# Optimization experiments

Hardware: AMD Instinct MI355X
Metric: run time of the kernel (lower is better)

## Reference

```python
import jax, jax.numpy as jnp
import numpy as np

HEADS, DIM_HEAD, CHUNK, GROUPS, EPS = 4, 32, 2048, 8, 1e-5


def setup_inputs() -> dict:
    key = jax.random.key(0)
    ks = jax.random.split(key, 10)
    B, C, H, W = 1, 128, 128, 128
    inner = HEADS * DIM_HEAD  # 128
    s = 0.02
    return {
        "x": jax.random.normal(ks[0], (B, C, H, W), jnp.float32),
        "w_qkv": jax.random.normal(ks[1], (3 * inner, C), jnp.float32) * s,
        "se_w1": jax.random.normal(ks[2], (inner // 4, inner), jnp.float32) * s,
        "se_b1": jax.random.normal(ks[3], (inner // 4,), jnp.float32) * s,
        "se_w2": jax.random.normal(ks[4], (inner, inner // 4), jnp.float32) * s,
        "se_b2": jax.random.normal(ks[5], (inner,), jnp.float32) * s,
        "out_w": jax.random.normal(ks[6], (C, inner), jnp.float32) * s,
        "out_b": jax.random.normal(ks[7], (C,), jnp.float32) * s,
        "gn_w": 1.0 + jax.random.normal(ks[8], (C,), jnp.float32) * s,
        "gn_b": jax.random.normal(ks[9], (C,), jnp.float32) * s,
    }


def reference(x, w_qkv, se_w1, se_b1, se_w2, se_b2, out_w, out_b, gn_w, gn_b):
    B, C, H, W = x.shape
    inner = HEADS * DIM_HEAD
    hw = H * W
    nc = hw // CHUNK  # hw chosen divisible by CHUNK
    scale = DIM_HEAD ** -0.5

    # 1x1 conv to qkv (no bias)
    qkv = jnp.einsum('oc,bchw->bohw', w_qkv, x)  # [B, 3*inner, H, W]
    q, k, v = jnp.split(qkv.reshape(B, 3 * inner, hw), 3, axis=1)

    def to_blocks(t):  # [B, inner, hw] -> [B*heads, dh, nc, CHUNK]
        return t.reshape(B * HEADS, DIM_HEAD, nc, CHUNK)

    q, k, v = to_blocks(q), to_blocks(k), to_blocks(v)

    # block-diagonal attention: attn[n, j] = softmax_j(q[:, n]^T k[:, j])
    attn = jax.nn.softmax(jnp.einsum('bdnc,bdne->bnce', q, k) * scale, axis=-1)
    # chunk_out[d, j] = sum_c v[d, c] * attn[c, j]  (contracts the un-normalized axis, as in torch bmm(v, attn))
    out = jnp.einsum('bdnc,bncj->bdnj', v, attn).reshape(B, inner, H, W)

    # SE gating
    s = out.mean(axis=(2, 3))                       # [B, inner]
    s = jax.nn.silu(s @ se_w1.T + se_b1)            # [B, inner//4]
    g = jax.nn.sigmoid(s @ se_w2.T + se_b2)         # [B, inner]
    out = out * g[:, :, None, None]

    # output 1x1 conv + GroupNorm(8, C)
    y = jnp.einsum('oc,bchw->bohw', out_w, out) + out_b[None, :, None, None]
    yg = y.reshape(B, GROUPS, C // GROUPS, H, W)
    mu = yg.mean(axis=(2, 3, 4), keepdims=True)
    var = yg.var(axis=(2, 3, 4), keepdims=True)
    yn = ((yg - mu) * jax.lax.rsqrt(var + EPS)).reshape(B, C, H, W)
    return yn * gn_w[None, :, None, None] + gn_b[None, :, None, None]
```

## Files before the change

### kernel.cpp

```cpp
#include <hip/hip_runtime.h>
#include <hip/hip_bf16.h>

#define HW 16384
#define QSCALE (0.17677669529663687f * 1.4426950408889634f)

typedef __attribute__((ext_vector_type(8))) short short8;
typedef __attribute__((ext_vector_type(4))) float floatx4;
typedef __attribute__((ext_vector_type(16))) float floatx16;

__device__ inline unsigned cvt_pk_bf16(float a, float b) {
  unsigned r;
  asm("v_cvt_pk_bf16_f32 %0, %1, %2" : "=v"(r) : "v"(a), "v"(b));
  return r;
}
__device__ inline unsigned short f2bf(float a) {
  return (unsigned short)(cvt_pk_bf16(a, 0.f) & 0xffff);
}
__device__ inline float bf2f(unsigned short u) {
  union { unsigned u; float f; } c;
  c.u = (unsigned)u << 16;
  return c.f;
}
__device__ inline void permlane32_swap(unsigned& a, unsigned& b) {
  asm("v_permlane32_swap_b32 %0, %1" : "+v"(a), "+v"(b));
}

__global__ __launch_bounds__(256) void cast_w(
    const float* __restrict__ w, unsigned short* __restrict__ w_bf) {
  const int i4 = (blockIdx.x * 256 + threadIdx.x) * 4;
  const int o = i4 >> 7;
  const float sc = (o < 128) ? QSCALE : 1.f;
  float4 v = *(const float4*)&w[i4];
  uint2 u = {cvt_pk_bf16(v.x * sc, v.y * sc), cvt_pk_bf16(v.z * sc, v.w * sc)};
  *(uint2*)&w_bf[i4] = u;
}

__global__ __launch_bounds__(256) void cast_transpose_x(
    const float* __restrict__ x, unsigned short* __restrict__ x_t) {
  __shared__ float tile[128][65];
  const int p0 = blockIdx.x * 64;
  const int t = threadIdx.x;
  #pragma unroll
  for (int i = 0; i < 32; ++i) {
    int idx = t + i * 256;
    int c = idx >> 6, p = idx & 63;
    tile[c][p] = x[c * HW + p0 + p];
  }
  __syncthreads();
  const int p = t >> 2, q = t & 3;
  unsigned u[16];
  #pragma unroll
  for (int i = 0; i < 16; ++i)
    u[i] = cvt_pk_bf16(tile[q * 32 + 2 * i][p], tile[q * 32 + 2 * i + 1][p]);
  unsigned short* dst = &x_t[(p0 + p) * 128 + q * 32];
  #pragma unroll
  for (int i = 0; i < 4; ++i) *(uint4*)&dst[i * 8] = *(const uint4*)&u[i * 4];
}

__global__ __launch_bounds__(512) void gemm_qkv(
    const unsigned short* __restrict__ w_bf, const unsigned short* __restrict__ x_t,
    unsigned short* __restrict__ q_t, unsigned short* __restrict__ k_t,
    unsigned short* __restrict__ v_bf) {
  const int wave = threadIdx.x >> 6, lane = threadIdx.x & 63;
  const int lr = lane & 15, g = lane >> 4;
  const int p0 = blockIdx.x * 64;
  const int ow = wave * 48;
  const floatx4 zero = {0.f, 0.f, 0.f, 0.f};

  short8 a[3][4];
  #pragma unroll
  for (int mf = 0; mf < 3; ++mf)
    #pragma unroll
    for (int kk = 0; kk < 4; ++kk)
      a[mf][kk] = *(const short8*)&w_bf[(ow + mf * 16 + lr) * 128 + kk * 32 + g * 8];

  floatx4 acc[3][4];
  #pragma unroll
  for (int mf = 0; mf < 3; ++mf)
    #pragma unroll
    for (int nf = 0; nf < 4; ++nf) acc[mf][nf] = zero;

  #pragma unroll
  for (int kk = 0; kk < 4; ++kk) {
    #pragma unroll
    for (int nf = 0; nf < 4; ++nf) {
      short8 b = *(const short8*)&x_t[(p0 + nf * 16 + lr) * 128 + kk * 32 + g * 8];
      #pragma unroll
      for (int mf = 0; mf < 3; ++mf)
        acc[mf][nf] = __builtin_amdgcn_mfma_f32_16x16x32_bf16(a[mf][kk], b, acc[mf][nf], 0, 0, 0);
    }
  }

  #pragma unroll
  for (int mf = 0; mf < 3; ++mf) {
    const int ob = ow + mf * 16;
    #pragma unroll
    for (int nf = 0; nf < 4; ++nf) {
      const int p = p0 + nf * 16 + lr;
      const int c = p & 2047, nn = p >> 11;
      floatx4 r = acc[mf][nf];
      if (ob < 128) {
        const int bh = ob >> 5, d0 = (ob & 31) + g * 4;
        uint2 u = {cvt_pk_bf16(r[0], r[1]), cvt_pk_bf16(r[2], r[3])};
        *(uint2*)&q_t[((bh * 8 + nn) * 2048 + c) * 32 + d0] = u;
      } else if (ob < 256) {
        const int oo = ob - 128, bh = oo >> 5, d0 = (oo & 31) + g * 4;
        uint2 u = {cvt_pk_bf16(r[0], r[1]), cvt_pk_bf16(r[2], r[3])};
        *(uint2*)&k_t[((bh * 8 + nn) * 2048 + c) * 32 + d0] = u;
      } else {
        const int d = ob - 256 + g * 4;
        #pragma unroll
        for (int rr = 0; rr < 4; ++rr) v_bf[(d + rr) * HW + p] = f2bf(r[rr]);
      }
    }
  }
}

__global__ __launch_bounds__(256) void row_mean_v(
    const unsigned short* __restrict__ v_bf, float* __restrict__ s) {
  const int ch = blockIdx.x;
  float sum = 0;
  for (int i = threadIdx.x; i < 2048; i += 256) {
    short8 u = *(const short8*)&v_bf[ch * HW + i * 8];
    #pragma unroll
    for (int k = 0; k < 8; ++k) sum += bf2f((unsigned short)u[k]);
  }
  __shared__ float red[256];
  red[threadIdx.x] = sum;
  __syncthreads();
  for (int st = 128; st > 0; st >>= 1) {
    if (threadIdx.x < st) red[threadIdx.x] += red[threadIdx.x + st];
    __syncthreads();
  }
  if (threadIdx.x == 0) s[ch] = red[0] * (1.f / HW);
}

__global__ __launch_bounds__(128) void se_mlp(
    const float* __restrict__ s, const float* __restrict__ w1,
    const float* __restrict__ b1, const float* __restrict__ w2,
    const float* __restrict__ b2, const float* __restrict__ out_w,
    unsigned short* __restrict__ w_g) {
  __shared__ float s_sh[128], s1_sh[32], g_sh[128];
  const int t = threadIdx.x;
  s_sh[t] = s[t];
  __syncthreads();
  if (t < 32) {
    float a = b1[t];
    for (int c = 0; c < 128; ++c) a += w1[t * 128 + c] * s_sh[c];
    s1_sh[t] = a / (1.f + __expf(-a));
  }
  __syncthreads();
  {
    float a = b2[t];
    for (int i = 0; i < 32; ++i) a += w2[t * 32 + i] * s1_sh[i];
    g_sh[t] = 1.f / (1.f + __expf(-a));
  }
  __syncthreads();
  for (int o = 0; o < 128; ++o) w_g[o * 128 + t] = f2bf(out_w[o * 128 + t] * g_sh[t]);
}

__global__ __launch_bounds__(256, 2) void attn_stats_mfma(
    const unsigned short* __restrict__ q_t, const unsigned short* __restrict__ k_t,
    float* __restrict__ zbuf) {
  const int wave = threadIdx.x >> 6, lane = threadIdx.x & 63;
  const int f = blockIdx.x;
  const int bn = (f >> 7) * 8 + (f & 7);
  const int ct = (f >> 3) & 15;
  const int l31 = lane & 31, h = lane >> 5;
  const int c0 = ct * 128 + wave * 32;
  const floatx16 z16 = {0.f,0.f,0.f,0.f,0.f,0.f,0.f,0.f,
                        0.f,0.f,0.f,0.f,0.f,0.f,0.f,0.f};

  const unsigned short* qp = &q_t[(bn * 2048 + c0 + l31) * 32 + h * 8];
  short8 aq0 = *(const short8*)qp;
  short8 aq1 = *(const short8*)(qp + 16);

  float z[16] = {};
  const unsigned short* kb = &k_t[(bn * 2048 + l31) * 32 + h * 8];

  short8 b0a = *(const short8*)&kb[0];
  short8 b0b = *(const short8*)&kb[16];
  short8 b1a = *(const short8*)&kb[32 * 32];
  short8 b1b = *(const short8*)&kb[32 * 32 + 16];

  for (int e0 = 0; e0 < 2048; e0 += 64) {
    const unsigned short* nk = &kb[(e0 + 64) * 32];
    short8 nb0a = *(const short8*)&nk[0];
    short8 nb0b = *(const short8*)&nk[16];
    short8 nb1a = *(const short8*)&nk[32 * 32];
    short8 nb1b = *(const short8*)&nk[32 * 32 + 16];

    floatx16 s1 = __builtin_amdgcn_mfma_f32_32x32x16_bf16(aq0, b0a, z16, 0, 0, 0);
    s1 = __builtin_amdgcn_mfma_f32_32x32x16_bf16(aq1, b0b, s1, 0, 0, 0);
    floatx16 s2 = __builtin_amdgcn_mfma_f32_32x32x16_bf16(aq0, b1a, z16, 0, 0, 0);
    s2 = __builtin_amdgcn_mfma_f32_32x32x16_bf16(aq1, b1b, s2, 0, 0, 0);
    #pragma unroll
    for (int r = 0; r < 16; ++r) z[r] += exp2f(s1[r]) + exp2f(s2[r]);

    b0a = nb0a; b0b = nb0b; b1a = nb1a; b1b = nb1b;
  }
  #pragma unroll
  for (int r = 0; r < 16; ++r) {
    float v = z[r];
    v += __shfl_xor(v, 1); v += __shfl_xor(v, 2); v += __shfl_xor(v, 4);
    v += __shfl_xor(v, 8); v += __shfl_xor(v, 16);
    z[r] = v;
  }
  if (l31 == 0) {
    #pragma unroll
    for (int r = 0; r < 16; ++r)
      zbuf[bn * 2048 + c0 + (r & 3) + 8 * (r >> 2) + 4 * h] = z[r];
  }
}

__global__ __launch_bounds__(256) void vz_cast(
    const unsigned short* __restrict__ v_bf, const float* __restrict__ zbuf,
    unsigned short* __restrict__ vz) {
  const int idx = (blockIdx.x * 256 + threadIdx.x) * 8;
  const int row = idx >> 14, p = idx & 16383;
  const int bh = row >> 5, nn = p >> 11, c = p & 2047;
  short8 v8 = *(const short8*)&v_bf[idx];
  const int zb = (bh * 8 + nn) * 2048 + c;
  float zs[8];
  #pragma unroll
  for (int i = 0; i < 8; ++i) zs[i] = __builtin_amdgcn_rcpf(zbuf[zb + i]);
  unsigned u[4];
  #pragma unroll
  for (int i = 0; i < 4; ++i)
    u[i] = cvt_pk_bf16(bf2f((unsigned short)v8[2 * i]) * zs[2 * i],
                       bf2f((unsigned short)v8[2 * i + 1]) * zs[2 * i + 1]);
  uint4 o = {u[0], u[1], u[2], u[3]};
  *(uint4*)&vz[idx] = o;
}

__global__ __launch_bounds__(256, 2) void attn_apply_mfma(
    const unsigned short* __restrict__ q_t, const unsigned short* __restrict__ k_t,
    const unsigned short* __restrict__ vz, unsigned short* __restrict__ att_t) {
  const int wave = threadIdx.x >> 6, lane = threadIdx.x & 63;
  const int f = blockIdx.x;
  const int bn = (f >> 7) * 8 + (f & 7);
  const int js = (f >> 3) & 7;
  const int chf = (f >> 6) & 1;
  const int bh = bn >> 3, nn = bn & 7;
  const int jA = js * 256 + wave * 64;
  const int jB = jA + 32;
  const int l31 = lane & 31, h = lane >> 5;
  const floatx16 z16 = {0.f,0.f,0.f,0.f,0.f,0.f,0.f,0.f,
                        0.f,0.f,0.f,0.f,0.f,0.f,0.f,0.f};

  const unsigned short* kpA = &k_t[(bn * 2048 + jA + l31) * 32 + h * 8];
  const unsigned short* kpB = &k_t[(bn * 2048 + jB + l31) * 32 + h * 8];
  short8 bkA0 = *(const short8*)kpA, bkA1 = *(const short8*)(kpA + 16);
  short8 bkB0 = *(const short8*)kpB, bkB1 = *(const short8*)(kpB + 16);

  floatx16 accA = z16, accB = z16;
  const unsigned short* qb = &q_t[(bn * 2048 + chf * 1024 + l31) * 32 + h * 8];
  const unsigned short* vb = &vz[(bh * 32 + l31) * HW + nn * 2048 + chf * 1024 + h * 8];

  short8 aq0 = *(const short8*)&qb[0];
  short8 aq1 = *(const short8*)&qb[16];
  short8 av0 = *(const short8*)&vb[0];
  short8 av1 = *(const short8*)&vb[16];

  for (int c0 = 0; c0 < 1024; c0 += 32) {
    short8 naq0 = *(const short8*)&qb[(c0 + 32) * 32];
    short8 naq1 = *(const short8*)&qb[(c0 + 32) * 32 + 16];
    short8 nav0 = *(const short8*)&vb[c0 + 32];
    short8 nav1 = *(const short8*)&vb[c0 + 48];

    {
      floatx16 s = __builtin_amdgcn_mfma_f32_32x32x16_bf16(aq0, bkA0, z16, 0, 0, 0);
      s = __builtin_amdgcn_mfma_f32_32x32x16_bf16(aq1, bkA1, s, 0, 0, 0);
      unsigned pk0 = cvt_pk_bf16(exp2f(s[0]),  exp2f(s[1]));
      unsigned pk1 = cvt_pk_bf16(exp2f(s[2]),  exp2f(s[3]));
      unsigned pk2 = cvt_pk_bf16(exp2f(s[4]),  exp2f(s[5]));
      unsigned pk3 = cvt_pk_bf16(exp2f(s[6]),  exp2f(s[7]));
      unsigned pk4 = cvt_pk_bf16(exp2f(s[8]),  exp2f(s[9]));
      unsigned pk5 = cvt_pk_bf16(exp2f(s[10]), exp2f(s[11]));
      unsigned pk6 = cvt_pk_bf16(exp2f(s[12]), exp2f(s[13]));
      unsigned pk7 = cvt_pk_bf16(exp2f(s[14]), exp2f(s[15]));
      permlane32_swap(pk0, pk2);
      permlane32_swap(pk1, pk3);
      permlane32_swap(pk4, pk6);
      permlane32_swap(pk5, pk7);
      union { uint4 u; short8 s8; } b0, b1;
      b0.u = make_uint4(pk0, pk1, pk2, pk3);
      b1.u = make_uint4(pk4, pk5, pk6, pk7);
      accA = __builtin_amdgcn_mfma_f32_32x32x16_bf16(av0, b0.s8, accA, 0, 0, 0);
      accA = __builtin_amdgcn_mfma_f32_32x32x16_bf16(av1, b1.s8, accA, 0, 0, 0);
    }
    {
      floatx16 s = __builtin_amdgcn_mfma_f32_32x32x16_bf16(aq0, bkB0, z16, 0, 0, 0);
      s = __builtin_amdgcn_mfma_f32_32x32x16_bf16(aq1, bkB1, s, 0, 0, 0);
      unsigned pk0 = cvt_pk_bf16(exp2f(s[0]),  exp2f(s[1]));
      unsigned pk1 = cvt_pk_bf16(exp2f(s[2]),  exp2f(s[3]));
      unsigned pk2 = cvt_pk_bf16(exp2f(s[4]),  exp2f(s[5]));
      unsigned pk3 = cvt_pk_bf16(exp2f(s[6]),  exp2f(s[7]));
      unsigned pk4 = cvt_pk_bf16(exp2f(s[8]),  exp2f(s[9]));
      unsigned pk5 = cvt_pk_bf16(exp2f(s[10]), exp2f(s[11]));
      unsigned pk6 = cvt_pk_bf16(exp2f(s[12]), exp2f(s[13]));
      unsigned pk7 = cvt_pk_bf16(exp2f(s[14]), exp2f(s[15]));
      permlane32_swap(pk0, pk2);
      permlane32_swap(pk1, pk3);
      permlane32_swap(pk4, pk6);
      permlane32_swap(pk5, pk7);
      union { uint4 u; short8 s8; } b0, b1;
      b0.u = make_uint4(pk0, pk1, pk2, pk3);
      b1.u = make_uint4(pk4, pk5, pk6, pk7);
      accB = __builtin_amdgcn_mfma_f32_32x32x16_bf16(av0, b0.s8, accB, 0, 0, 0);
      accB = __builtin_amdgcn_mfma_f32_32x32x16_bf16(av1, b1.s8, accB, 0, 0, 0);
    }
    aq0 = naq0; aq1 = naq1; av0 = nav0; av1 = nav1;
  }

  unsigned short* orowA = att_t + chf * 2097152 +
                          (nn * 2048 + jA + l31) * 128 + bh * 32 + 4 * h;
  unsigned short* orowB = att_t + chf * 2097152 +
                          (nn * 2048 + jB + l31) * 128 + bh * 32 + 4 * h;
  #pragma unroll
  for (int q = 0; q < 4; ++q) {
    uint2 uA = {cvt_pk_bf16(accA[4 * q], accA[4 * q + 1]),
                cvt_pk_bf16(accA[4 * q + 2], accA[4 * q + 3])};
    *(uint2*)&orowA[q * 8] = uA;
    uint2 uB = {cvt_pk_bf16(accB[4 * q], accB[4 * q + 1]),
                cvt_pk_bf16(accB[4 * q + 2], accB[4 * q + 3])};
    *(uint2*)&orowB[q * 8] = uB;
  }
}

__global__ __launch_bounds__(256) void gemm_out(
    const unsigned short* __restrict__ w_g, const unsigned short* __restrict__ att_t,
    const float* __restrict__ out_b, unsigned short* __restrict__ ybuf_bf,
    float* __restrict__ part) {
  const int wave = threadIdx.x >> 6, lane = threadIdx.x & 63;
  const int lr = lane & 15, g = lane >> 4;
  const int p0 = blockIdx.x * 64;
  const int o0 = wave * 32;
  const floatx4 zero = {0.f, 0.f, 0.f, 0.f};

  short8 a[2][4];
  #pragma unroll
  for (int mf = 0; mf < 2; ++mf)
    #pragma unroll
    for (int kk = 0; kk < 4; ++kk)
      a[mf][kk] = *(const short8*)&w_g[(o0 + mf * 16 + lr) * 128 + kk * 32 + g * 8];

  floatx4 acc[2][4];
  #pragma unroll
  for (int mf = 0; mf < 2; ++mf)
    #pragma unroll
    for (int nf = 0; nf < 4; ++nf) acc[mf][nf] = zero;

  #pragma unroll
  for (int ks = 0; ks < 8; ++ks) {
    const unsigned short* att = att_t + (ks >> 2) * 2097152;
    const int kk = ks & 3;
    #pragma unroll
    for (int nf = 0; nf < 4; ++nf) {
      short8 b = *(const short8*)&att[(p0 + nf * 16 + lr) * 128 + kk * 32 + g * 8];
      acc[0][nf] = __builtin_amdgcn_mfma_f32_16x16x32_bf16(a[0][kk], b, acc[0][nf], 0, 0, 0);
      acc[1][nf] = __builtin_amdgcn_mfma_f32_16x16x32_bf16(a[1][kk], b, acc[1][nf], 0, 0, 0);
    }
  }

  float sg[2] = {0.f, 0.f}, ssg[2] = {0.f, 0.f};
  #pragma unroll
  for (int mf = 0; mf < 2; ++mf) {
    #pragma unroll
    for (int nf = 0; nf < 4; ++nf) {
      #pragma unroll
      for (int r = 0; r < 4; ++r) {
        const int o = o0 + mf * 16 + g * 4 + r;
        float y = acc[mf][nf][r] + out_b[o];
        ybuf_bf[o * HW + p0 + nf * 16 + lr] = f2bf(y);
        sg[mf] += y;
        ssg[mf] += y * y;
      }
    }
  }
  #pragma unroll
  for (int mf = 0; mf < 2; ++mf) {
    float a1 = sg[mf], a2 = ssg[mf];
    #pragma unroll
    for (int st = 1; st < 64; st <<= 1) {
      a1 += __shfl_xor(a1, st);
      a2 += __shfl_xor(a2, st);
    }
    if (lane == 0) {
      part[(blockIdx.x * 8 + wave * 2 + mf) * 2 + 0] = a1;
      part[(blockIdx.x * 8 + wave * 2 + mf) * 2 + 1] = a2;
    }
  }
}

__global__ __launch_bounds__(256) void gn_finalize(
    const float* __restrict__ part, float* __restrict__ stat) {
  const int gg = blockIdx.x;
  const int t = threadIdx.x;
  __shared__ float r1[256], r2[256];
  r1[t] = part[(t * 8 + gg) * 2 + 0];
  r2[t] = part[(t * 8 + gg) * 2 + 1];
  __syncthreads();
  for (int st = 128; st > 0; st >>= 1) {
    if (t < st) { r1[t] += r1[t + st]; r2[t] += r2[t + st]; }
    __syncthreads();
  }
  if (t == 0) {
    const float inv_n = 1.f / (16.f * HW);
    float mu = r1[0] * inv_n;
    float var = r2[0] * inv_n - mu * mu;
    stat[gg * 2 + 0] = mu;
    stat[gg * 2 + 1] = rsqrtf(var + 1e-5f);
  }
}

__global__ __launch_bounds__(256) void gn_apply(
    const unsigned short* __restrict__ ybuf_bf, const float* __restrict__ stat,
    const float* __restrict__ gn_w, const float* __restrict__ gn_b,
    float* __restrict__ outp) {
  const int i = (blockIdx.x * 256 + threadIdx.x) * 8;
  const int ch = i >> 14;
  const int g = ch >> 4;
  float mu = stat[g * 2], rs = stat[g * 2 + 1];
  float w = gn_w[ch] * rs;
  float b = gn_b[ch] - mu * w;
  short8 v = *(const short8*)&ybuf_bf[i];
  float4 r0 = {bf2f((unsigned short)v[0]) * w + b, bf2f((unsigned short)v[1]) * w + b,
               bf2f((unsigned short)v[2]) * w + b, bf2f((unsigned short)v[3]) * w + b};
  float4 r1 = {bf2f((unsigned short)v[4]) * w + b, bf2f((unsigned short)v[5]) * w + b,
               bf2f((unsigned short)v[6]) * w + b, bf2f((unsigned short)v[7]) * w + b};
  *(float4*)&outp[i] = r0;
  *(float4*)&outp[i + 4] = r1;
}

extern "C" void kernel_launch(void* const* d_in, const int* in_sizes, int n_in,
                              void* d_out, int out_size, void* d_ws, size_t ws_size,
                              hipStream_t stream) {
  const float* x     = (const float*)d_in[0];
  const float* w_qkv = (const float*)d_in[1];
  const float* se_w1 = (const float*)d_in[2];
  const float* se_b1 = (const float*)d_in[3];
  const float* se_w2 = (const float*)d_in[4];
  const float* se_b2 = (const float*)d_in[5];
  const float* out_w = (const float*)d_in[6];
  const float* out_b = (const float*)d_in[7];
  const float* gn_w  = (const float*)d_in[8];
  const float* gn_b  = (const float*)d_in[9];
  float* out = (float*)d_out;

  float* ws = (float*)d_ws;
  float* zbuf  = ws;
  float* se_s  = zbuf + 65536;
  float* part  = se_s + 128;
  float* stat  = part + 4096;
  unsigned short* w_bf    = (unsigned short*)(stat + 16);
  unsigned short* x_t     = w_bf + 49152;
  unsigned short* q_t     = x_t + 2097152;
  unsigned short* k_t     = q_t + 2097152;
  unsigned short* v_bf    = k_t + 2097152;
  unsigned short* vz      = v_bf + 2097152;
  unsigned short* w_g     = vz + 2097152;
  unsigned short* att_t   = w_g + 16384;
  unsigned short* ybuf_bf = att_t + 4194304;

  cast_w<<<48, 256, 0, stream>>>(w_qkv, w_bf);
  cast_transpose_x<<<256, 256, 0, stream>>>(x, x_t);
  gemm_qkv<<<256, 512, 0, stream>>>(w_bf, x_t, q_t, k_t, v_bf);
  row_mean_v<<<128, 256, 0, stream>>>(v_bf, se_s);
  se_mlp<<<1, 128, 0, stream>>>(se_s, se_w1, se_b1, se_w2, se_b2, out_w, w_g);
  attn_stats_mfma<<<512, 256, 0, stream>>>(q_t, k_t, zbuf);
  vz_cast<<<1024, 256, 0, stream>>>(v_bf, zbuf, vz);
  attn_apply_mfma<<<512, 256, 0, stream>>>(q_t, k_t, vz, att_t);
  gemm_out<<<256, 256, 0, stream>>>(w_g, att_t, out_b, ybuf_bf, part);
  gn_finalize<<<8, 256, 0, stream>>>(part, stat);
  gn_apply<<<1024, 256, 0, stream>>>(ybuf_bf, stat, gn_w, gn_b, out);
}
```

Baseline: 136.5 us.

## Split attention reductions four ways to raise grid parallelism

The softmax-denominator kernel now splits the key axis into four partial sums, which vz_cast adds together. The apply kernel splits the contracted c axis into four partial outputs instead of two, and gemm_out accumulates all four. Grid sizes grow (2048 and 1024 blocks) and launch bounds allow four blocks per CU, so more waves run on the 256 CUs. In exchange, att_t workspace doubles, gemm_out reads twice as much data, and four more zpart loads are needed per element.

```diff
diff --git a/kernel.cpp b/kernel.cpp
--- a/kernel.cpp
+++ b/kernel.cpp
@@ -159,13 +159,14 @@
   for (int o = 0; o < 128; ++o) w_g[o * 128 + t] = f2bf(out_w[o * 128 + t] * g_sh[t]);
 }
 
-__global__ __launch_bounds__(256, 2) void attn_stats_mfma(
+__global__ __launch_bounds__(256, 4) void attn_stats_mfma(
     const unsigned short* __restrict__ q_t, const unsigned short* __restrict__ k_t,
-    float* __restrict__ zbuf) {
+    float* __restrict__ zpart) {
   const int wave = threadIdx.x >> 6, lane = threadIdx.x & 63;
   const int f = blockIdx.x;
-  const int bn = (f >> 7) * 8 + (f & 7);
+  const int bn = ((f >> 7) & 3) * 8 + (f & 7);
   const int ct = (f >> 3) & 15;
+  const int epart = f >> 9;
   const int l31 = lane & 31, h = lane >> 5;
   const int c0 = ct * 128 + wave * 32;
   const floatx16 z16 = {0.f,0.f,0.f,0.f,0.f,0.f,0.f,0.f,
@@ -176,14 +177,14 @@
   short8 aq1 = *(const short8*)(qp + 16);
 
   float z[16] = {};
-  const unsigned short* kb = &k_t[(bn * 2048 + l31) * 32 + h * 8];
+  const unsigned short* kb = &k_t[(bn * 2048 + epart * 512 + l31) * 32 + h * 8];
 
   short8 b0a = *(const short8*)&kb[0];
   short8 b0b = *(const short8*)&kb[16];
   short8 b1a = *(const short8*)&kb[32 * 32];
   short8 b1b = *(const short8*)&kb[32 * 32 + 16];
 
-  for (int e0 = 0; e0 < 2048; e0 += 64) {
+  for (int e0 = 0; e0 < 512; e0 += 64) {
     const unsigned short* nk = &kb[(e0 + 64) * 32];
     short8 nb0a = *(const short8*)&nk[0];
     short8 nb0b = *(const short8*)&nk[16];
@@ -209,12 +210,12 @@
   if (l31 == 0) {
     #pragma unroll
     for (int r = 0; r < 16; ++r)
-      zbuf[bn * 2048 + c0 + (r & 3) + 8 * (r >> 2) + 4 * h] = z[r];
+      zpart[epart * 65536 + bn * 2048 + c0 + (r & 3) + 8 * (r >> 2) + 4 * h] = z[r];
   }
 }
 
 __global__ __launch_bounds__(256) void vz_cast(
-    const unsigned short* __restrict__ v_bf, const float* __restrict__ zbuf,
+    const unsigned short* __restrict__ v_bf, const float* __restrict__ zpart,
     unsigned short* __restrict__ vz) {
   const int idx = (blockIdx.x * 256 + threadIdx.x) * 8;
   const int row = idx >> 14, p = idx & 16383;
@@ -223,7 +224,9 @@
   const int zb = (bh * 8 + nn) * 2048 + c;
   float zs[8];
   #pragma unroll
-  for (int i = 0; i < 8; ++i) zs[i] = __builtin_amdgcn_rcpf(zbuf[zb + i]);
+  for (int i = 0; i < 8; ++i)
+    zs[i] = __builtin_amdgcn_rcpf((zpart[zb + i] + zpart[65536 + zb + i]) +
+                                  (zpart[131072 + zb + i] + zpart[196608 + zb + i]));
   unsigned u[4];
   #pragma unroll
   for (int i = 0; i < 4; ++i)
@@ -233,16 +236,16 @@
   *(uint4*)&vz[idx] = o;
 }
 
-__global__ __launch_bounds__(256, 2) void attn_apply_mfma(
+__global__ __launch_bounds__(256, 4) void attn_apply_mfma(
     const unsigned short* __restrict__ q_t, const unsigned short* __restrict__ k_t,
     const unsigned short* __restrict__ vz, unsigned short* __restrict__ att_t) {
   const int wave = threadIdx.x >> 6, lane = threadIdx.x & 63;
   const int f = blockIdx.x;
-  const int bn = (f >> 7) * 8 + (f & 7);
-  const int js = (f >> 3) & 7;
-  const int chf = (f >> 6) & 1;
+  const int bn = ((f >> 6) & 3) * 8 + (f & 7);
+  const int jg = (f >> 3) & 7;
+  const int cpart = f >> 8;
   const int bh = bn >> 3, nn = bn & 7;
-  const int jA = js * 256 + wave * 64;
+  const int jA = jg * 256 + wave * 64;
   const int jB = jA + 32;
   const int l31 = lane & 31, h = lane >> 5;
   const floatx16 z16 = {0.f,0.f,0.f,0.f,0.f,0.f,0.f,0.f,
@@ -254,15 +257,15 @@
   short8 bkB0 = *(const short8*)kpB, bkB1 = *(const short8*)(kpB + 16);
 
   floatx16 accA = z16, accB = z16;
-  const unsigned short* qb = &q_t[(bn * 2048 + chf * 1024 + l31) * 32 + h * 8];
-  const unsigned short* vb = &vz[(bh * 32 + l31) * HW + nn * 2048 + chf * 1024 + h * 8];
+  const unsigned short* qb = &q_t[(bn * 2048 + cpart * 512 + l31) * 32 + h * 8];
+  const unsigned short* vb = &vz[(bh * 32 + l31) * HW + nn * 2048 + cpart * 512 + h * 8];
 
   short8 aq0 = *(const short8*)&qb[0];
   short8 aq1 = *(const short8*)&qb[16];
   short8 av0 = *(const short8*)&vb[0];
   short8 av1 = *(const short8*)&vb[16];
 
-  for (int c0 = 0; c0 < 1024; c0 += 32) {
+  for (int c0 = 0; c0 < 512; c0 += 32) {
     short8 naq0 = *(const short8*)&qb[(c0 + 32) * 32];
     short8 naq1 = *(const short8*)&qb[(c0 + 32) * 32 + 16];
     short8 nav0 = *(const short8*)&vb[c0 + 32];
@@ -313,9 +316,9 @@
     aq0 = naq0; aq1 = naq1; av0 = nav0; av1 = nav1;
   }
 
-  unsigned short* orowA = att_t + chf * 2097152 +
+  unsigned short* orowA = att_t + cpart * 2097152 +
                           (nn * 2048 + jA + l31) * 128 + bh * 32 + 4 * h;
-  unsigned short* orowB = att_t + chf * 2097152 +
+  unsigned short* orowB = att_t + cpart * 2097152 +
                           (nn * 2048 + jB + l31) * 128 + bh * 32 + 4 * h;
   #pragma unroll
   for (int q = 0; q < 4; ++q) {
@@ -352,7 +355,7 @@
     for (int nf = 0; nf < 4; ++nf) acc[mf][nf] = zero;
 
   #pragma unroll
-  for (int ks = 0; ks < 8; ++ks) {
+  for (int ks = 0; ks < 16; ++ks) {
     const unsigned short* att = att_t + (ks >> 2) * 2097152;
     const int kk = ks & 3;
     #pragma unroll
@@ -449,8 +452,8 @@
   float* out = (float*)d_out;
 
   float* ws = (float*)d_ws;
-  float* zbuf  = ws;
-  float* se_s  = zbuf + 65536;
+  float* zpart = ws;
+  float* se_s  = zpart + 262144;
   float* part  = se_s + 128;
   float* stat  = part + 4096;
   unsigned short* w_bf    = (unsigned short*)(stat + 16);
@@ -461,16 +464,16 @@
   unsigned short* vz      = v_bf + 2097152;
   unsigned short* w_g     = vz + 2097152;
   unsigned short* att_t   = w_g + 16384;
-  unsigned short* ybuf_bf = att_t + 4194304;
+  unsigned short* ybuf_bf = att_t + 8388608;
 
   cast_w<<<48, 256, 0, stream>>>(w_qkv, w_bf);
   cast_transpose_x<<<256, 256, 0, stream>>>(x, x_t);
   gemm_qkv<<<256, 512, 0, stream>>>(w_bf, x_t, q_t, k_t, v_bf);
   row_mean_v<<<128, 256, 0, stream>>>(v_bf, se_s);
   se_mlp<<<1, 128, 0, stream>>>(se_s, se_w1, se_b1, se_w2, se_b2, out_w, w_g);
-  attn_stats_mfma<<<512, 256, 0, stream>>>(q_t, k_t, zbuf);
-  vz_cast<<<1024, 256, 0, stream>>>(v_bf, zbuf, vz);
-  attn_apply_mfma<<<512, 256, 0, stream>>>(q_t, k_t, vz, att_t);
+  attn_stats_mfma<<<2048, 256, 0, stream>>>(q_t, k_t, zpart);
+  vz_cast<<<1024, 256, 0, stream>>>(v_bf, zpart, vz);
+  attn_apply_mfma<<<1024, 256, 0, stream>>>(q_t, k_t, vz, att_t);
   gemm_out<<<256, 256, 0, stream>>>(w_g, att_t, out_b, ybuf_bf, part);
   gn_finalize<<<8, 256, 0, stream>>>(part, stat);
   gn_apply<<<1024, 256, 0, stream>>>(ybuf_bf, stat, gn_w, gn_b, out);
```

After: 134.5 us. About the same (-1.4%).
